# Kernel optimization log

Hardware: AMD Instinct MI355X
Metric: run time of the kernel (lower is better)

Reference implementation:

```python
import jax, jax.numpy as jnp
import numpy as np

B, T, C = 4, 2048, 1024
H = 16
HS = C // H          # 64
FF = 4 * C           # 4096
EPS = 1e-5


def layernorm(x, g, b):
    mu = jnp.mean(x, axis=-1, keepdims=True)
    var = jnp.mean(jnp.square(x - mu), axis=-1, keepdims=True)
    return (x - mu) * jax.lax.rsqrt(var + EPS) * g + b


def setup_inputs() -> dict:
    key = jax.random.key(0)
    ks = jax.random.split(key, 16)
    s_in = 1.0 / np.sqrt(C)
    s_ff = 1.0 / np.sqrt(FF)
    return {
        "x": jax.random.normal(ks[0], (B, T, C), jnp.float32),
        # per-head Q/K/V projections stacked: [H, C, HS]
        "Wq": jax.random.normal(ks[1], (H, C, HS), jnp.float32) * s_in,
        "Wk": jax.random.normal(ks[2], (H, C, HS), jnp.float32) * s_in,
        "Wv": jax.random.normal(ks[3], (H, C, HS), jnp.float32) * s_in,
        "Wproj": jax.random.normal(ks[4], (C, C), jnp.float32) * s_in,
        "bproj": jnp.zeros((C,), jnp.float32),
        "W1": jax.random.normal(ks[5], (C, FF), jnp.float32) * s_in,
        "b1": jnp.zeros((FF,), jnp.float32),
        "W2": jax.random.normal(ks[6], (FF, C), jnp.float32) * s_ff,
        "b2": jnp.zeros((C,), jnp.float32),
        "ln1_g": jnp.ones((C,), jnp.float32),
        "ln1_b": jnp.zeros((C,), jnp.float32),
        "ln2_g": jnp.ones((C,), jnp.float32),
        "ln2_b": jnp.zeros((C,), jnp.float32),
    }


def reference(x, Wq, Wk, Wv, Wproj, bproj, W1, b1, W2, b2,
              ln1_g, ln1_b, ln2_g, ln2_b):
    # --- multi-head causal self-attention on layernorm1(x) ---
    h = layernorm(x, ln1_g, ln1_b)                       # [B,T,C]
    q = jnp.einsum('btc,hcd->bhtd', h, Wq)
    k = jnp.einsum('btc,hcd->bhtd', h, Wk)
    v = jnp.einsum('btc,hcd->bhtd', h, Wv)
    scores = jnp.einsum('bhtd,bhsd->bhts', q, k) * (HS ** -0.5)
    causal = jnp.tril(jnp.ones((T, T), bool))
    scores = jnp.where(causal, scores, -jnp.inf)
    att = jax.nn.softmax(scores, axis=-1)                # [B,H,T,T]
    o = jnp.einsum('bhts,bhsd->bthd', att, v).reshape(B, T, C)  # head concat
    x = x + o @ Wproj + bproj
    # --- feedforward on layernorm2(x) ---
    h2 = layernorm(x, ln2_g, ln2_b)
    ff = jax.nn.relu(h2 @ W1 + b1) @ W2 + b2
    return x + ff
```

## Files before the change

kernel.cpp:

```cpp
#include <hip/hip_runtime.h>
#include <cstddef>
#include <cstdio>

#define Bn   4
#define Tn   2048
#define Cn   1024
#define Hn   16
#define HSn  64
#define FFn  4096
#define ROWS (Bn*Tn)
#define QKVW (3*Cn)

typedef __attribute__((ext_vector_type(8))) __bf16 bf16x8;
typedef __attribute__((ext_vector_type(4))) float f32x4;

__device__ __forceinline__ unsigned short f2bf(float f){
  unsigned int u = __float_as_uint(f);
  unsigned int r = (u + 0x7fffu + ((u >> 16) & 1u)) >> 16;
  return (unsigned short)r;
}

#define GLD16(g, l) __builtin_amdgcn_global_load_lds( \
    (__attribute__((address_space(1))) void*)(void*)(g), \
    (__attribute__((address_space(3))) void*)(l), 16, 0, 0)

__device__ __forceinline__ float wave_sum_f(float v){
#pragma unroll
  for (int o = 32; o > 0; o >>= 1) v += __shfl_xor(v, o);
  return v;
}

__global__ void ln_bf16(const float* __restrict__ x, const float* __restrict__ g,
                        const float* __restrict__ bb, unsigned short* __restrict__ y){
  const int row = blockIdx.x;
  const int tid = threadIdx.x;
  const float4 v = reinterpret_cast<const float4*>(x + (size_t)row * Cn)[tid];
  float s  = v.x + v.y + v.z + v.w;
  float ss = v.x*v.x + v.y*v.y + v.z*v.z + v.w*v.w;
  s = wave_sum_f(s); ss = wave_sum_f(ss);
  __shared__ float sm[4], sm2[4];
  const int w = tid >> 6, lane = tid & 63;
  if (lane == 0){ sm[w] = s; sm2[w] = ss; }
  __syncthreads();
  const float tot  = sm[0] + sm[1] + sm[2] + sm[3];
  const float tot2 = sm2[0] + sm2[1] + sm2[2] + sm2[3];
  const float mu = tot * (1.0f / Cn);
  const float rs = rsqrtf(tot2 * (1.0f / Cn) - mu * mu + 1e-5f);
  const float4 gv = reinterpret_cast<const float4*>(g)[tid];
  const float4 bv = reinterpret_cast<const float4*>(bb)[tid];
  ushort4 o;
  o.x = f2bf((v.x - mu) * rs * gv.x + bv.x);
  o.y = f2bf((v.y - mu) * rs * gv.y + bv.y);
  o.z = f2bf((v.z - mu) * rs * gv.z + bv.z);
  o.w = f2bf((v.w - mu) * rs * gv.w + bv.w);
  reinterpret_cast<ushort4*>(y + (size_t)row * Cn)[tid] = o;
}

__global__ void transpose_cast(const float* __restrict__ in, unsigned short* __restrict__ out,
                               int R, int Cc){
  __shared__ float t[64][65];
  const int tid = threadIdx.x;
  const int r0 = blockIdx.y * 64, c0 = blockIdx.x * 64;
  const int rb = tid >> 6, cl = tid & 63;
#pragma unroll
  for (int j = 0; j < 16; ++j)
    t[rb + j*4][cl] = in[(size_t)(r0 + rb + j*4) * Cc + c0 + cl];
  __syncthreads();
#pragma unroll
  for (int j = 0; j < 16; ++j)
    out[(size_t)(c0 + rb + j*4) * R + r0 + cl] = f2bf(t[cl][rb + j*4]);
}

__global__ void repack_qkv_t(const float* __restrict__ Wq, const float* __restrict__ Wk,
                             const float* __restrict__ Wv, unsigned short* __restrict__ Wrt){
  __shared__ float t[64][65];
  const int tid = threadIdx.x;
  const int kb = blockIdx.x * 64;
  const int hh = blockIdx.y;
  const int sec = hh >> 4, h = hh & 15;
  const float* W = (sec == 0) ? Wq : ((sec == 1) ? Wk : Wv);
  const int rb = tid >> 6, dl = tid & 63;
#pragma unroll
  for (int j = 0; j < 16; ++j)
    t[rb + j*4][dl] = W[h * (Cn*HSn) + (size_t)(kb + rb + j*4) * HSn + dl];
  __syncthreads();
#pragma unroll
  for (int j = 0; j < 16; ++j)
    Wrt[(size_t)(sec*Cn + h*64 + rb + j*4) * Cn + kb + dl] = f2bf(t[dl][rb + j*4]);
}

template<int RELU, int OUT_BF16>
__global__ __launch_bounds__(512, 2)
void gemm256(const unsigned short* __restrict__ A, const unsigned short* __restrict__ Bt,
             void* __restrict__ Cout, int M, int N, int K,
             const float* __restrict__ bias, const float* __restrict__ resid){
  __shared__ __align__(16) unsigned short As[4 * 8192];
  __shared__ __align__(16) unsigned short Bs[4 * 8192];
  const int tid  = threadIdx.x;
  const int wid  = tid >> 6, lane = tid & 63;
  const int wm   = wid >> 2, wn = wid & 3;
  const int fr   = lane & 15, Lq = lane >> 4;

  const int id  = blockIdx.x + gridDim.x * blockIdx.y;
  const int Nbn = gridDim.x;
  const int cpx = (gridDim.x * gridDim.y) >> 3;
  const int wg  = (id & 7) * cpx + (id >> 3);
  const int bm  = wg / Nbn;
  const int bn  = wg - bm * Nbn;

  const int srow  = wid * 8 + (lane >> 3);
  const int skoff = (((lane & 7) ^ (srow & 7)) * 8);
  const unsigned short* Abase = A  + (size_t)(bm * 256 + srow) * K + skoff;
  const unsigned short* Bbase = Bt + (size_t)(bn * 256 + srow) * K + skoff;

  auto stA = [&](int t, int h){
    const unsigned short* g0 = Abase + (size_t)h * 128 * K + (size_t)t * 64;
    unsigned short* l0 = As + (((2*t + h) & 3) * 8192) + wid * 512;
    GLD16(g0, l0);
    GLD16(g0 + (size_t)64 * K, l0 + 4096);
  };
  auto stB = [&](int t, int h){
    const unsigned short* g0 = Bbase + (size_t)h * 128 * K + (size_t)t * 64;
    unsigned short* l0 = Bs + (((2*t + h) & 3) * 8192) + wid * 512;
    GLD16(g0, l0);
    GLD16(g0 + (size_t)64 * K, l0 + 4096);
  };

  f32x4 acc[8][4] = {};
  const int NT = K >> 6;

  stA(0, 0); stA(0, 1); stB(0, 0); stB(0, 1);

  for (int t = 0; t < NT; ++t){
    const unsigned short* aS = As + (((2*t + wm) & 3) * 8192);
    const unsigned short* bS = Bs + (((2*t + (wn >> 1)) & 3) * 8192)
                                  + ((wn & 1) * 64) * 64;
    const bool pf = (t + 1 < NT);

    if (pf){ stA(t+1, 0); stA(t+1, 1); stB(t+1, 0); stB(t+1, 1); }
    __builtin_amdgcn_sched_barrier(0);
    if (pf) asm volatile("s_waitcnt vmcnt(8)");
    else    asm volatile("s_waitcnt vmcnt(0)");
    __builtin_amdgcn_s_barrier();

#pragma unroll
    for (int kk = 0; kk < 2; ++kk){
      const int kx = (((kk*4) + Lq) ^ (fr & 7)) * 8;
      bf16x8 bfv[4], af[4];
#pragma unroll
      for (int ni = 0; ni < 4; ++ni)
        bfv[ni] = *reinterpret_cast<const bf16x8*>(&bS[(ni*16 + fr) * 64 + kx]);
#pragma unroll
      for (int m2 = 0; m2 < 4; ++m2)
        af[m2] = *reinterpret_cast<const bf16x8*>(&aS[(m2*16 + fr) * 64 + kx]);
#pragma unroll
      for (int m2 = 0; m2 < 4; ++m2)
#pragma unroll
        for (int ni = 0; ni < 4; ++ni)
          acc[m2][ni] = __builtin_amdgcn_mfma_f32_16x16x32_bf16(
              af[m2], bfv[ni], acc[m2][ni], 0, 0, 0);
#pragma unroll
      for (int m2 = 0; m2 < 4; ++m2)
        af[m2] = *reinterpret_cast<const bf16x8*>(&aS[((4+m2)*16 + fr) * 64 + kx]);
#pragma unroll
      for (int m2 = 0; m2 < 4; ++m2)
#pragma unroll
        for (int ni = 0; ni < 4; ++ni)
          acc[4+m2][ni] = __builtin_amdgcn_mfma_f32_16x16x32_bf16(
              af[m2], bfv[ni], acc[4+m2][ni], 0, 0, 0);
    }
    __builtin_amdgcn_sched_barrier(0);
    __builtin_amdgcn_s_barrier();
  }

  const int lc = fr, lr4 = Lq * 4;
#pragma unroll
  for (int ni = 0; ni < 4; ++ni){
    const int col = bn*256 + wn*64 + ni*16 + lc;
    const float bv = bias ? bias[col] : 0.f;
#pragma unroll
    for (int mi = 0; mi < 8; ++mi){
      const int rowb = bm*256 + wm*128 + mi*16 + lr4;
#pragma unroll
      for (int r = 0; r < 4; ++r){
        float v = acc[mi][ni][r] + bv;
        if (RELU) v = fmaxf(v, 0.f);
        if (resid) v += resid[(size_t)(rowb + r) * N + col];
        if (OUT_BF16)
          ((unsigned short*)Cout)[(size_t)(rowb + r) * N + col] = f2bf(v);
        else
          ((float*)Cout)[(size_t)(rowb + r) * N + col] = v;
      }
    }
  }
}

template<int RELU, int OUT_BF16>
__global__ __launch_bounds__(256)
void gemm_mfma(const unsigned short* __restrict__ A, const unsigned short* __restrict__ Bt,
               void* __restrict__ Cout, int M, int N, int K,
               const float* __restrict__ bias, const float* __restrict__ resid){
  __shared__ __align__(16) unsigned short As[128*32];
  __shared__ __align__(16) unsigned short Bs[128*32];
  const int tid = threadIdx.x;
  const int wave = tid >> 6, lane = tid & 63;
  const int wm = wave >> 1, wn = wave & 1;

  const int id = blockIdx.x + gridDim.x * blockIdx.y;
  const int Nbn = gridDim.x;
  const int xcd = id & 7;
  const int sidx = id >> 3;
  const int pm = sidx / Nbn;
  const int bm = xcd + 8 * pm;
  const int bn = sidx - pm * Nbn;

  const int srow = lane >> 2;
  const int row0 = wave*16 + srow;
  const int sw = (((lane & 3) ^ ((row0 >> 1) & 3)) * 8);
  const unsigned short* Ag0 = A  + (size_t)(bm*128 + row0) * K + sw;
  const unsigned short* Bg0 = Bt + (size_t)(bn*128 + row0) * K + sw;
  unsigned short* AsW0 = As + (wave*16) * 32;
  unsigned short* AsW1 = As + (wave*16 + 64) * 32;
  unsigned short* BsW0 = Bs + (wave*16) * 32;
  unsigned short* BsW1 = Bs + (wave*16 + 64) * 32;

  f32x4 acc[4][4] = {};

  const int fr = lane & 15;
  const int Lq = lane >> 4;
  const int fx = ((Lq ^ ((fr >> 1) & 3)) * 8);

  for (int kt = 0; kt < K; kt += 32){
    __syncthreads();
    GLD16(Ag0 + kt,                AsW0);
    GLD16(Ag0 + (size_t)64*K + kt, AsW1);
    GLD16(Bg0 + kt,                BsW0);
    GLD16(Bg0 + (size_t)64*K + kt, BsW1);
    __syncthreads();

    bf16x8 af[4], bfv[4];
#pragma unroll
    for (int mi = 0; mi < 4; ++mi)
      af[mi] = *reinterpret_cast<const bf16x8*>(&As[(wm*64 + mi*16 + fr) * 32 + fx]);
#pragma unroll
    for (int ni = 0; ni < 4; ++ni)
      bfv[ni] = *reinterpret_cast<const bf16x8*>(&Bs[(wn*64 + ni*16 + fr) * 32 + fx]);
#pragma unroll
    for (int mi = 0; mi < 4; ++mi)
#pragma unroll
      for (int ni = 0; ni < 4; ++ni)
        acc[mi][ni] = __builtin_amdgcn_mfma_f32_16x16x32_bf16(
            af[mi], bfv[ni], acc[mi][ni], 0, 0, 0);
  }

  const int lc = lane & 15, lr4 = (lane >> 4) * 4;
#pragma unroll
  for (int ni = 0; ni < 4; ++ni){
    const int col = bn*128 + wn*64 + ni*16 + lc;
    const float bv = bias ? bias[col] : 0.f;
#pragma unroll
    for (int mi = 0; mi < 4; ++mi){
      const int rowb = bm*128 + wm*64 + mi*16 + lr4;
#pragma unroll
      for (int r = 0; r < 4; ++r){
        float v = acc[mi][ni][r] + bv;
        if (RELU) v = fmaxf(v, 0.f);
        if (resid) v += resid[(size_t)(rowb + r) * N + col];
        if (OUT_BF16)
          ((unsigned short*)Cout)[(size_t)(rowb + r) * N + col] = f2bf(v);
        else
          ((float*)Cout)[(size_t)(rowb + r) * N + col] = v;
      }
    }
  }
}

__global__ void blockify_kv(const unsigned short* __restrict__ qkv,
                            unsigned short* __restrict__ Kb,
                            unsigned short* __restrict__ Vb){
  const int st = blockIdx.x, h = blockIdx.y, b = blockIdx.z;
  const int tid = threadIdx.x;
  const size_t base = ((size_t)(b*Hn + h)*32 + st) * 4096;
#pragma unroll
  for (int it = 0; it < 2; ++it){
    const int idx = it*256 + tid;
    const int s = idx >> 3, d8 = idx & 7;
    const uint4 v = *reinterpret_cast<const uint4*>(
        qkv + (size_t)(b*Tn + st*64 + s)*QKVW + Cn + h*64 + d8*8);
    *reinterpret_cast<uint4*>(Kb + base + d8*512 + ((s ^ d8) * 8)) = v;
  }
#pragma unroll
  for (int it = 0; it < 2; ++it){
    const int idx = it*256 + tid;
    const int d = idx & 63, s8 = idx >> 6;
    unsigned short tmp[8];
#pragma unroll
    for (int j = 0; j < 8; ++j)
      tmp[j] = qkv[(size_t)(b*Tn + st*64 + s8*8 + j)*QKVW + 2*Cn + h*64 + d];
    ushort4 lo, hi;
    lo.x = tmp[0]; lo.y = tmp[1]; lo.z = tmp[2]; lo.w = tmp[3];
    hi.x = tmp[4]; hi.y = tmp[5]; hi.z = tmp[6]; hi.w = tmp[7];
    *reinterpret_cast<ushort4*>(Vb + base + s8*512 + ((d ^ s8) * 8))     = lo;
    *reinterpret_cast<ushort4*>(Vb + base + s8*512 + ((d ^ s8) * 8) + 4) = hi;
  }
}

__global__ __launch_bounds__(512, 2)
void attn_mfma3(const unsigned short* __restrict__ qkv,
                const unsigned short* __restrict__ Kb,
                const unsigned short* __restrict__ Vb,
                unsigned short* __restrict__ O){
  __shared__ __align__(16) unsigned short Kls[2][4096];
  __shared__ __align__(16) unsigned short Vls[2][4096];
  __shared__ __align__(16) unsigned short Pt[8][16][72];

  const int bh = blockIdx.x;
  const int b = bh >> 4, h = bh & 15;
  const int pg = blockIdx.y;
  const int tid = threadIdx.x;
  const int wv = tid >> 6, l = tid & 63;
  const int strip = (wv < 4) ? pg : (7 - pg);
  const int qblk = strip*4 + (wv & 3);
  const int Lq = l >> 4, fr = l & 15;
  const int maxst = (7 - pg)*4 + 3;

  const size_t kvbase = ((size_t)(b*Hn + h) * 32) * 4096;

  union U { uint4 u; bf16x8 v; };
  U qf[4][2];
  const unsigned short* Qbase = qkv + ((size_t)(b*Tn + qblk*64)) * QKVW + h*64;
#pragma unroll
  for (int f = 0; f < 4; ++f){
    const unsigned short* qr = Qbase + (size_t)(f*16 + fr) * QKVW + Lq*8;
    qf[f][0].u = *reinterpret_cast<const uint4*>(qr);
    qf[f][1].u = *reinterpret_cast<const uint4*>(qr + 32);
  }

  f32x4 Oa[4][4] = {};
  float lsum[4] = {0.f, 0.f, 0.f, 0.f};
  const float C1 = 0.18033688011112042f;
  const float C2 = 28.853900817779268f;

  auto stage = [&](int st, int buf){
    const unsigned short* gk = Kb + kvbase + (size_t)st*4096 + wv*512 + l*8;
    const unsigned short* gv = Vb + kvbase + (size_t)st*4096 + wv*512 + l*8;
    GLD16(gk, &Kls[buf][wv*512]);
    GLD16(gv, &Vls[buf][wv*512]);
  };

  stage(0, 0);

  for (int st = 0; st <= maxst; ++st){
    const int buf = st & 1;
    __syncthreads();
    if (st < maxst) stage(st + 1, buf ^ 1);
    if (st > qblk) continue;

    U k0[4], k1[4];
#pragma unroll
    for (int sb = 0; sb < 4; ++sb){
      const int s = sb*16 + fr;
      k0[sb].u = *reinterpret_cast<const uint4*>(&Kls[buf][ Lq   *512 + ((s ^  Lq   ) * 8)]);
      k1[sb].u = *reinterpret_cast<const uint4*>(&Kls[buf][(4+Lq)*512 + ((s ^ (4+Lq)) * 8)]);
    }
    U v0[4], v1[4];
#pragma unroll
    for (int db = 0; db < 4; ++db){
      const int d = db*16 + fr;
      v0[db].u = *reinterpret_cast<const uint4*>(&Vls[buf][ Lq   *512 + ((d ^  Lq   ) * 8)]);
      v1[db].u = *reinterpret_cast<const uint4*>(&Vls[buf][(4+Lq)*512 + ((d ^ (4+Lq)) * 8)]);
    }

    const bool diag = (st == qblk);
#pragma unroll
    for (int f = 0; f < 4; ++f){
      f32x4 S[4];
#pragma unroll
      for (int sb = 0; sb < 4; ++sb){
        f32x4 z = {0.f, 0.f, 0.f, 0.f};
        z     = __builtin_amdgcn_mfma_f32_16x16x32_bf16(k0[sb].v, qf[f][0].v, z, 0, 0, 0);
        S[sb] = __builtin_amdgcn_mfma_f32_16x16x32_bf16(k1[sb].v, qf[f][1].v, z, 0, 0, 0);
      }
#pragma unroll
      for (int sb = 0; sb < 4; ++sb){
        float p0 = exp2f(fmaf(S[sb][0], C1, -C2));
        float p1 = exp2f(fmaf(S[sb][1], C1, -C2));
        float p2 = exp2f(fmaf(S[sb][2], C1, -C2));
        float p3 = exp2f(fmaf(S[sb][3], C1, -C2));
        if (diag){
          const int s0 = sb*16 + Lq*4, q = f*16 + fr;
          if (s0 + 0 > q) p0 = 0.f;
          if (s0 + 1 > q) p1 = 0.f;
          if (s0 + 2 > q) p2 = 0.f;
          if (s0 + 3 > q) p3 = 0.f;
        }
        lsum[f] += (p0 + p1) + (p2 + p3);
        const unsigned int pk0 = (unsigned int)f2bf(p0) | ((unsigned int)f2bf(p1) << 16);
        const unsigned int pk1 = (unsigned int)f2bf(p2) | ((unsigned int)f2bf(p3) << 16);
        *reinterpret_cast<uint2*>(&Pt[wv][fr][sb*16 + Lq*4]) = make_uint2(pk0, pk1);
      }
      U pf0, pf1;
      pf0.u = *reinterpret_cast<const uint4*>(&Pt[wv][fr][Lq*8]);
      pf1.u = *reinterpret_cast<const uint4*>(&Pt[wv][fr][32 + Lq*8]);
#pragma unroll
      for (int db = 0; db < 4; ++db){
        Oa[db][f] = __builtin_amdgcn_mfma_f32_16x16x32_bf16(v0[db].v, pf0.v, Oa[db][f], 0, 0, 0);
        Oa[db][f] = __builtin_amdgcn_mfma_f32_16x16x32_bf16(v1[db].v, pf1.v, Oa[db][f], 0, 0, 0);
      }
    }
  }

#pragma unroll
  for (int f = 0; f < 4; ++f){
    float s = lsum[f];
    s += __shfl_xor(s, 16);
    s += __shfl_xor(s, 32);
    const float inv = 1.0f / s;
    const size_t orow = (size_t)(b*Tn + qblk*64 + f*16 + fr);
#pragma unroll
    for (int db = 0; db < 4; ++db){
      ushort4 o;
      o.x = f2bf(Oa[db][f][0] * inv);
      o.y = f2bf(Oa[db][f][1] * inv);
      o.z = f2bf(Oa[db][f][2] * inv);
      o.w = f2bf(Oa[db][f][3] * inv);
      *reinterpret_cast<ushort4*>(&O[orow*Cn + h*64 + db*16 + Lq*4]) = o;
    }
  }
}

extern "C" void kernel_launch(void* const* d_in, const int* in_sizes, int n_in,
                              void* d_out, int out_size, void* d_ws, size_t ws_size,
                              hipStream_t stream){
  const float* x     = (const float*)d_in[0];
  const float* Wq    = (const float*)d_in[1];
  const float* Wk    = (const float*)d_in[2];
  const float* Wv    = (const float*)d_in[3];
  const float* Wproj = (const float*)d_in[4];
  const float* bproj = (const float*)d_in[5];
  const float* W1    = (const float*)d_in[6];
  const float* b1    = (const float*)d_in[7];
  const float* W2    = (const float*)d_in[8];
  const float* b2    = (const float*)d_in[9];
  const float* ln1_g = (const float*)d_in[10];
  const float* ln1_b = (const float*)d_in[11];
  const float* ln2_g = (const float*)d_in[12];
  const float* ln2_b = (const float*)d_in[13];
  float* out = (float*)d_out;

  const size_t MB = 1024ull * 1024ull;
  if (ws_size < 192ull * MB){
    fprintf(stderr, "kernel_launch: need 192MB workspace, got %zu\n", ws_size);
    return;
  }
  char* ws = (char*)d_ws;
  float*          x1    = (float*)(ws + 0);
  unsigned short* h     = (unsigned short*)(ws + 32 * MB);
  unsigned short* qkvb  = (unsigned short*)(ws + 48 * MB);
  unsigned short* ff1   = (unsigned short*)(ws + 48 * MB);
  unsigned short* Kb    = (unsigned short*)(ws + 96 * MB);
  unsigned short* Vb    = (unsigned short*)(ws + 112 * MB);
  unsigned short* Ob    = (unsigned short*)(ws + 128 * MB);
  unsigned short* Wrt   = (unsigned short*)(ws + 144 * MB);
  unsigned short* Wpt   = (unsigned short*)(ws + 150 * MB);
  unsigned short* W1t   = (unsigned short*)(ws + 152 * MB);
  unsigned short* W2t   = (unsigned short*)(ws + 160 * MB);

  repack_qkv_t<<<dim3(Cn/64, 3*Hn), 256, 0, stream>>>(Wq, Wk, Wv, Wrt);
  transpose_cast<<<dim3(Cn/64,  Cn/64),  256, 0, stream>>>(Wproj, Wpt, Cn,  Cn);
  transpose_cast<<<dim3(FFn/64, Cn/64),  256, 0, stream>>>(W1,    W1t, Cn,  FFn);
  transpose_cast<<<dim3(Cn/64,  FFn/64), 256, 0, stream>>>(W2,    W2t, FFn, Cn);

  ln_bf16<<<ROWS, 256, 0, stream>>>(x, ln1_g, ln1_b, h);
  gemm256<0,1><<<dim3(QKVW/256, ROWS/256), 512, 0, stream>>>(
      h, Wrt, qkvb, ROWS, QKVW, Cn, nullptr, nullptr);
  blockify_kv<<<dim3(Tn/64, Hn, Bn), 256, 0, stream>>>(qkvb, Kb, Vb);
  attn_mfma3<<<dim3(64, 4), 512, 0, stream>>>(qkvb, Kb, Vb, Ob);
  gemm_mfma<0,0><<<dim3(Cn/128, ROWS/128), 256, 0, stream>>>(
      Ob, Wpt, x1, ROWS, Cn, Cn, bproj, x);
  ln_bf16<<<ROWS, 256, 0, stream>>>(x1, ln2_g, ln2_b, h);
  gemm256<1,1><<<dim3(FFn/256, ROWS/256), 512, 0, stream>>>(
      h, W1t, ff1, ROWS, FFn, Cn, b1, nullptr);
  gemm_mfma<0,0><<<dim3(Cn/128, ROWS/128), 256, 0, stream>>>(
      ff1, W2t, out, ROWS, Cn, FFn, b2, x1);
}
```

Before: 581.3 us.

## Double-buffer LDS in 128x128 GEMM with BK=64 and prefetch ring

Replaces the single-buffered BK=32 128x128 GEMM, used for the projection and FF2 GEMMs, with a two-stage LDS ring at BK=64. The next k-tile is prefetched with global_load_lds while the current one feeds MFMA, using a partial vmcnt wait and one barrier per tile. Block-to-XCD mapping is changed to a contiguous chunk per XCD, and the swizzle is widened to 8 lanes. LDS use doubles to 64KB per block, which with launch_bounds(256,2) may limit occupancy.

```diff
diff --git a/kernel.cpp b/kernel.cpp
--- a/kernel.cpp
+++ b/kernel.cpp
@@ -196,64 +196,82 @@
 }
 
 template<int RELU, int OUT_BF16>
-__global__ __launch_bounds__(256)
-void gemm_mfma(const unsigned short* __restrict__ A, const unsigned short* __restrict__ Bt,
-               void* __restrict__ Cout, int M, int N, int K,
-               const float* __restrict__ bias, const float* __restrict__ resid){
-  __shared__ __align__(16) unsigned short As[128*32];
-  __shared__ __align__(16) unsigned short Bs[128*32];
-  const int tid = threadIdx.x;
+__global__ __launch_bounds__(256, 2)
+void gemm128ring(const unsigned short* __restrict__ A, const unsigned short* __restrict__ Bt,
+                 void* __restrict__ Cout, int M, int N, int K,
+                 const float* __restrict__ bias, const float* __restrict__ resid){
+  __shared__ __align__(16) unsigned short As[2 * 8192];
+  __shared__ __align__(16) unsigned short Bs[2 * 8192];
+  const int tid  = threadIdx.x;
   const int wave = tid >> 6, lane = tid & 63;
-  const int wm = wave >> 1, wn = wave & 1;
-
-  const int id = blockIdx.x + gridDim.x * blockIdx.y;
+  const int wm   = wave >> 1, wn = wave & 1;
+  const int fr   = lane & 15, Lq = lane >> 4;
+
+  const int id  = blockIdx.x + gridDim.x * blockIdx.y;
   const int Nbn = gridDim.x;
-  const int xcd = id & 7;
-  const int sidx = id >> 3;
-  const int pm = sidx / Nbn;
-  const int bm = xcd + 8 * pm;
-  const int bn = sidx - pm * Nbn;
-
-  const int srow = lane >> 2;
-  const int row0 = wave*16 + srow;
-  const int sw = (((lane & 3) ^ ((row0 >> 1) & 3)) * 8);
-  const unsigned short* Ag0 = A  + (size_t)(bm*128 + row0) * K + sw;
-  const unsigned short* Bg0 = Bt + (size_t)(bn*128 + row0) * K + sw;
-  unsigned short* AsW0 = As + (wave*16) * 32;
-  unsigned short* AsW1 = As + (wave*16 + 64) * 32;
-  unsigned short* BsW0 = Bs + (wave*16) * 32;
-  unsigned short* BsW1 = Bs + (wave*16 + 64) * 32;
+  const int cpx = (gridDim.x * gridDim.y) >> 3;
+  const int wg  = (id & 7) * cpx + (id >> 3);
+  const int bm  = wg / Nbn;
+  const int bn  = wg - bm * Nbn;
+
+  const int srow  = tid >> 3;
+  const int skoff = (((tid & 7) ^ (srow & 7)) * 8);
+  const unsigned short* Abase = A  + (size_t)(bm * 128 + srow) * K + skoff;
+  const unsigned short* Bbase = Bt + (size_t)(bn * 128 + srow) * K + skoff;
+
+  auto stA = [&](int t){
+    const unsigned short* g0 = Abase + (size_t)t * 64;
+    unsigned short* l0 = As + ((t & 1) * 8192) + tid * 8;
+#pragma unroll
+    for (int j = 0; j < 4; ++j)
+      GLD16(g0 + (size_t)(j*32) * K, l0 + j*2048);
+  };
+  auto stB = [&](int t){
+    const unsigned short* g0 = Bbase + (size_t)t * 64;
+    unsigned short* l0 = Bs + ((t & 1) * 8192) + tid * 8;
+#pragma unroll
+    for (int j = 0; j < 4; ++j)
+      GLD16(g0 + (size_t)(j*32) * K, l0 + j*2048);
+  };
 
   f32x4 acc[4][4] = {};
-
-  const int fr = lane & 15;
-  const int Lq = lane >> 4;
-  const int fx = ((Lq ^ ((fr >> 1) & 3)) * 8);
-
-  for (int kt = 0; kt < K; kt += 32){
-    __syncthreads();
-    GLD16(Ag0 + kt,                AsW0);
-    GLD16(Ag0 + (size_t)64*K + kt, AsW1);
-    GLD16(Bg0 + kt,                BsW0);
-    GLD16(Bg0 + (size_t)64*K + kt, BsW1);
-    __syncthreads();
-
-    bf16x8 af[4], bfv[4];
-#pragma unroll
-    for (int mi = 0; mi < 4; ++mi)
-      af[mi] = *reinterpret_cast<const bf16x8*>(&As[(wm*64 + mi*16 + fr) * 32 + fx]);
-#pragma unroll
-    for (int ni = 0; ni < 4; ++ni)
-      bfv[ni] = *reinterpret_cast<const bf16x8*>(&Bs[(wn*64 + ni*16 + fr) * 32 + fx]);
-#pragma unroll
-    for (int mi = 0; mi < 4; ++mi)
+  const int NT = K >> 6;
+
+  stA(0); stB(0);
+
+  for (int t = 0; t < NT; ++t){
+    const unsigned short* aS = As + ((t & 1) * 8192);
+    const unsigned short* bS = Bs + ((t & 1) * 8192);
+    const bool pf = (t + 1 < NT);
+
+    if (pf){ stA(t+1); stB(t+1); }
+    __builtin_amdgcn_sched_barrier(0);
+    if (pf) asm volatile("s_waitcnt vmcnt(8)");
+    else    asm volatile("s_waitcnt vmcnt(0)");
+    __builtin_amdgcn_s_barrier();
+
+#pragma unroll
+    for (int kk = 0; kk < 2; ++kk){
+      const int kx = (((kk*4) + Lq) ^ (fr & 7)) * 8;
+      bf16x8 bfv[4], af[4];
 #pragma unroll
       for (int ni = 0; ni < 4; ++ni)
-        acc[mi][ni] = __builtin_amdgcn_mfma_f32_16x16x32_bf16(
-            af[mi], bfv[ni], acc[mi][ni], 0, 0, 0);
-  }
-
-  const int lc = lane & 15, lr4 = (lane >> 4) * 4;
+        bfv[ni] = *reinterpret_cast<const bf16x8*>(&bS[(wn*64 + ni*16 + fr) * 64 + kx]);
+#pragma unroll
+      for (int mi = 0; mi < 4; ++mi)
+        af[mi] = *reinterpret_cast<const bf16x8*>(&aS[(wm*64 + mi*16 + fr) * 64 + kx]);
+#pragma unroll
+      for (int mi = 0; mi < 4; ++mi)
+#pragma unroll
+        for (int ni = 0; ni < 4; ++ni)
+          acc[mi][ni] = __builtin_amdgcn_mfma_f32_16x16x32_bf16(
+              af[mi], bfv[ni], acc[mi][ni], 0, 0, 0);
+    }
+    __builtin_amdgcn_sched_barrier(0);
+    __builtin_amdgcn_s_barrier();
+  }
+
+  const int lc = fr, lr4 = Lq * 4;
 #pragma unroll
   for (int ni = 0; ni < 4; ++ni){
     const int col = bn*128 + wn*64 + ni*16 + lc;
@@ -476,11 +494,11 @@
       h, Wrt, qkvb, ROWS, QKVW, Cn, nullptr, nullptr);
   blockify_kv<<<dim3(Tn/64, Hn, Bn), 256, 0, stream>>>(qkvb, Kb, Vb);
   attn_mfma3<<<dim3(64, 4), 512, 0, stream>>>(qkvb, Kb, Vb, Ob);
-  gemm_mfma<0,0><<<dim3(Cn/128, ROWS/128), 256, 0, stream>>>(
+  gemm128ring<0,0><<<dim3(Cn/128, ROWS/128), 256, 0, stream>>>(
       Ob, Wpt, x1, ROWS, Cn, Cn, bproj, x);
   ln_bf16<<<ROWS, 256, 0, stream>>>(x1, ln2_g, ln2_b, h);
   gemm256<1,1><<<dim3(FFn/256, ROWS/256), 512, 0, stream>>>(
       h, W1t, ff1, ROWS, FFn, Cn, b1, nullptr);
-  gemm_mfma<0,0><<<dim3(Cn/128, ROWS/128), 256, 0, stream>>>(
+  gemm128ring<0,0><<<dim3(Cn/128, ROWS/128), 256, 0, stream>>>(
       ff1, W2t, out, ROWS, Cn, FFn, b2, x1);
 }
```

New measurement: 546.9 us. -5.9%, faster.
